# Performance work log

Hardware: AMD Instinct MI355X
Metric: run time of the kernel (lower is better)

Reference implementation:

```python
import jax, jax.numpy as jnp
import numpy as np

BS = 16; N_PER = 1024; N = BS * N_PER; K = 9; E = N * K
H = 128; NODE_D = 64; EDGE_D = 16; RBF_DIM = 20; R_CUT = 1.0; L = 4; SF = 0.1


def setup_inputs():
    ks = jax.random.split(jax.random.key(0), 24)
    X = jax.random.normal(ks[0], (N, 3), dtype=jnp.float32) * 0.5
    node_attr = jax.random.normal(ks[1], (N, NODE_D), dtype=jnp.float32)
    edge_attr = jax.random.normal(ks[2], (E, EDGE_D), dtype=jnp.float32)
    idx = jnp.arange(N, dtype=jnp.int32)
    bid = idx // N_PER
    Seg = ((idx % N_PER) >= (N_PER // 2)).astype(jnp.int32)
    row = jnp.repeat(idx, K)
    col = (row // N_PER) * N_PER + jax.random.randint(ks[3], (E,), 0, N_PER, dtype=jnp.int32)
    edges = jnp.stack([row, col])

    def g(k, shape, fan):
        return jax.random.normal(k, shape, dtype=jnp.float32) * (1.0 / float(np.sqrt(fan)))

    MI = 2 * H + RBF_DIM + EDGE_D  # message MLP input dim
    return {
        'X': X, 'node_attr': node_attr, 'edge_attr': edge_attr,
        'W_in1': g(ks[4], (NODE_D, H), NODE_D), 'b_in1': jnp.zeros((H,), jnp.float32),
        'W_in2': g(ks[5], (H, H), H), 'b_in2': jnp.zeros((H,), jnp.float32),
        'We1': g(ks[6], (L, MI, H), MI), 'be1': jnp.zeros((L, H), jnp.float32),
        'We2': g(ks[7], (L, H, H), H), 'be2': jnp.zeros((L, H), jnp.float32),
        'Wv': g(ks[8], (L, H, H), H), 'Wvv': g(ks[9], (L, H, H), H),
        'Wh1': g(ks[10], (L, 2 * H, H), 2 * H), 'bh1': jnp.zeros((L, H), jnp.float32),
        'Wh2': g(ks[11], (L, H, H), H), 'bh2': jnp.zeros((L, H), jnp.float32),
        'Wi1': g(ks[12], (L, H, H), H), 'bi1': jnp.zeros((L, H), jnp.float32),
        'Wi2': g(ks[13], (L, H, H), H), 'bi2': jnp.zeros((L, H), jnp.float32),
        'Wgv1': g(ks[14], (H, H), H), 'Wgv2': g(ks[15], (H, H), H),
        'Wg1': g(ks[16], (2 * H, H), 2 * H), 'bg1': jnp.zeros((H,), jnp.float32),
        'Wg2': g(ks[17], (H, 2 * H), H), 'bg2': jnp.zeros((2 * H,), jnp.float32),
        'Wf': g(ks[18], (H, 9), H),
        'edges': edges, 'Seg': Seg, 'bid': bid,
    }


def _fwd(X, node_attr, edge_attr, W_in1, b_in1, W_in2, b_in2, We1, be1, We2, be2, Wv, Wvv, Wh1, bh1, Wh2, bh2, Wi1, bi1, Wi2, bi2, Wgv1, Wgv2, Wg1, bg1, Wg2, bg2, Wf, edges, Seg, bid):
    silu = jax.nn.silu
    row, col = edges[0], edges[1]
    nseg = 2 * BS
    seg_id = bid * 2 + Seg  # (complex, receptor/ligand) segment id
    # coord2radial + Bessel RBF with cosine cutoff
    diff = X[row] - X[col]
    norm = jnp.sqrt(jnp.sum(diff * diff, axis=-1)) + 1e-8
    unit = diff / norm[:, None]
    freqs = jnp.arange(1, RBF_DIM + 1, dtype=X.dtype) * (jnp.pi / R_CUT)
    rbf = jnp.sin(norm[:, None] * freqs[None, :]) / norm[:, None]
    cut = 0.5 * (jnp.cos(jnp.pi * jnp.clip(norm, 0.0, R_CUT) / R_CUT) + 1.0)
    rbf = rbf * cut[:, None]
    # in_conv
    h = silu(node_attr @ W_in1 + b_in1) @ W_in2 + b_in2
    v = jnp.zeros((N, H, 3), dtype=h.dtype)
    counts = jax.ops.segment_sum(jnp.ones((N,), dtype=h.dtype), seg_id, num_segments=nseg)
    opp = bid * 2 + (1 - Seg)  # opposite-molecule segment per node
    for i in range(L):
        # PINN message passing (PaiNN-style equivariant layer)
        m_in = jnp.concatenate([h[row], h[col], rbf, edge_attr], axis=-1)
        m = silu(m_in @ We1[i] + be1[i]) @ We2[i] + be2[i]  # [E, H]
        agg = jax.ops.segment_sum(m, row, num_segments=N)
        h_intra = h + silu(jnp.concatenate([h, agg], axis=-1) @ Wh1[i] + bh1[i]) @ Wh2[i] + bh2[i]
        v_msg = (m @ Wv[i])[:, :, None] * unit[:, None, :] + (m @ Wvv[i])[:, :, None] * v[col]
        v = v + jax.ops.segment_sum(v_msg, row, num_segments=N)
        # cross receptor<->ligand softmax attention: (H_a @ H_b.T).mean(1) == H_a @ mean(H_b)
        mean_h = jax.ops.segment_sum(h_intra, seg_id, num_segments=nseg) / counts[:, None]
        score = jnp.sum(h_intra * mean_h[opp], axis=-1)
        smax = jax.ops.segment_max(score, seg_id, num_segments=nseg)
        ex = jnp.exp(score - smax[seg_id])
        w = ex / jax.ops.segment_sum(ex, seg_id, num_segments=nseg)[seg_id]
        gated = h_intra * w[:, None]
        h = h_intra + silu(gated @ Wi1[i] + bi1[i]) @ Wi2[i] + bi2[i]
    # gated equivariant block
    v1 = jnp.einsum('nhc,hk->nkc', v, Wgv1)
    v2 = jnp.einsum('nhc,hk->nkc', v, Wgv2)
    v2n = jnp.sqrt(jnp.sum(v2 * v2, axis=-1) + 1e-8)
    mix = silu(jnp.concatenate([h, v2n], axis=-1) @ Wg1 + bg1) @ Wg2 + bg2
    h, bgate = mix[:, :H], mix[:, H:]
    v = v1 * bgate[:, :, None]
    # final_conv + per-(complex, molecule) pooled prediction vectors [2*BS, 9, 3]
    pv = jnp.einsum('nhc,ho->noc', v * h[:, :, None], Wf)
    pred = jax.ops.segment_sum(pv.reshape(N, 27), seg_id, num_segments=nseg).reshape(nseg, 9, 3)
    # kron/outer-product quadratic surface params: A [., 3, 3], b [., 3]
    A = (pred[:, 0, :, None] * pred[:, 1, None, :] + pred[:, 3, :, None] * pred[:, 2, None, :]
         + pred[:, 4, :, None] * pred[:, 5, None, :] + pred[:, 7, :, None] * pred[:, 6, None, :]) / (SF * SF)
    bvec = pred[:, 8] / SF
    return jnp.concatenate([A, bvec[:, :, None]], axis=2)  # [2*BS, 3, 4]


def reference(X, node_attr, edge_attr, W_in1, b_in1, W_in2, b_in2, We1, be1, We2, be2, Wv, Wvv, Wh1, bh1, Wh2, bh2, Wi1, bi1, Wi2, bi2, Wgv1, Wgv2, Wg1, bg1, Wg2, bg2, Wf, edges, Seg, bid):
    return _fwd(X, node_attr, edge_attr, W_in1, b_in1, W_in2, b_in2, We1, be1, We2, be2, Wv, Wvv, Wh1, bh1, Wh2, bh2, Wi1, bi1, Wi2, bi2, Wgv1, Wgv2, Wg1, bg1, Wg2, bg2, Wf, edges, Seg, bid)
```

## Files before the change

kernel.cpp:

```cpp
#include <hip/hip_runtime.h>
#include <math.h>

#define NN 16384
#define NE 147456
#define NSEGS 32
#define HD 128
#define RBF_D 20
#define EDGE_DD 16
#define NODE_DD 64
#define NLAYER 4
#define PI_F 3.14159265358979323846f


typedef __attribute__((ext_vector_type(8))) short v8s;
typedef __attribute__((ext_vector_type(4))) float v4f;
typedef __attribute__((ext_vector_type(8))) unsigned short v8u;

__device__ __forceinline__ unsigned short f2bf(float f) {
  union { float f; unsigned int u; } x; x.f = f;
  unsigned int u = x.u;
  return (unsigned short)((u + 0x7FFFu + ((u >> 16) & 1u)) >> 16);
}
__device__ __forceinline__ float bf2f(unsigned short b) {
  union { unsigned int u; float f; } x; x.u = ((unsigned int)b) << 16; return x.f;
}
__device__ __forceinline__ void split8(float4 a, float4 b, v8u& hi, v8u& lo) {
  float v[8] = {a.x, a.y, a.z, a.w, b.x, b.y, b.z, b.w};
#pragma unroll
  for (int i = 0; i < 8; i++) {
    unsigned short h = f2bf(v[i]);
    hi[i] = h;
    lo[i] = f2bf(v[i] - bf2f(h));
  }
}
__device__ __forceinline__ float silu_f(float v) { return v / (1.f + expf(-v)); }

struct WDesc { const float* src; const float* src2; unsigned short* hi; unsigned short* lo;
               int K; int N; int Kp; int ld; };
struct WDescs { WDesc d[48]; };
__global__ void wconv_k(WDescs ds) {
  WDesc d = ds.d[blockIdx.y];
  int idx = blockIdx.x * 256 + threadIdx.x;
  if (idx >= d.N * d.Kp) return;
  int n = idx / d.Kp, k = idx - n * d.Kp;
  const float* s = d.src; int nn = n;
  if (d.src2 && n >= 128) { s = d.src2; nn = n - 128; }
  float v = (k < d.K) ? s[(size_t)k * d.ld + nn] : 0.f;
  unsigned short h = f2bf(v);
  d.hi[idx] = h;
  d.lo[idx] = f2bf(v - bf2f(h));
}

__global__ void wcomb_k(const float* __restrict__ We2, const float* __restrict__ Wv,
                        const float* __restrict__ Wvv, float* __restrict__ Wc) {
  int l = blockIdx.z, which = blockIdx.y, xb = blockIdx.x;
  const float* A = We2 + (size_t)l * 128 * 128;
  const float* B = (which ? Wvv : Wv) + (size_t)l * 128 * 128;
  float* D = Wc + ((size_t)(which * NLAYER + l)) * 128 * 128;
  int n = threadIdx.x & 127, r2 = threadIdx.x >> 7;
#pragma unroll
  for (int i = 0; i < 8; i++) {
    int k1 = xb * 16 + r2 * 8 + i;
    float s = 0.f;
    for (int j = 0; j < 128; j++) s += A[k1 * 128 + j] * B[j * 128 + n];
    D[(size_t)k1 * 128 + n] = s;
  }
}
__global__ void bcomb_k(const float* __restrict__ be2, const float* __restrict__ Wv,
                        const float* __restrict__ Wvv, const float* __restrict__ be1,
                        float* __restrict__ bcv, float* __restrict__ bcvv,
                        float* __restrict__ b9, float* __restrict__ bx) {
  int l = blockIdx.x, n = threadIdx.x;
  const float* b = be2 + l * 128;
  float sv = 0.f, svv = 0.f;
  for (int j = 0; j < 128; j++) {
    sv  += b[j] * Wv[(size_t)l * 16384 + j * 128 + n];
    svv += b[j] * Wvv[(size_t)l * 16384 + j * 128 + n];
  }
  bcv[l * 128 + n] = sv; bcvv[l * 128 + n] = svv; b9[l * 128 + n] = 9.f * b[n];
  bx[l * 256 + n] = be1[l * 128 + n]; bx[l * 256 + 128 + n] = 0.f;
}

constexpr int LDS_S = 40;

template<int BM, int AMODE, int OUTM, int RESM>
__global__ __launch_bounds__(256, 2)
void mgemm_k(const float* A0f, const unsigned short* Ah0, const unsigned short* Al0,
             const unsigned short* __restrict__ Wth, const unsigned short* __restrict__ Wtl,
             int Kp, const float* __restrict__ bias, const float* __restrict__ resf,
             float* Cf, int ldc, unsigned short* Ch, unsigned short* Cl, int lda)
{
  constexpr int MT = BM / 32;
  __shared__ unsigned short Ah[BM * LDS_S], Al[BM * LDS_S];
  __shared__ unsigned short Bh[128 * LDS_S], Bl[128 * LDS_S];
  const int tid = threadIdx.x;
  const int m0 = blockIdx.x * BM;
  const int coff = blockIdx.y * 128;
  const int w = tid >> 6, lane = tid & 63;
  const int lm = lane & 15, kq = lane >> 4;
  const int wm = (w >> 1) * (BM / 2);
  const int wn = (w & 1) * 64;

  v4f acc[MT][4];
#pragma unroll
  for (int i = 0; i < MT; i++)
#pragma unroll
    for (int j = 0; j < 4; j++) acc[i][j] = (v4f){0.f, 0.f, 0.f, 0.f};

  const int KT = Kp >> 5;
  for (int kt = 0; kt < KT; kt++) {
#pragma unroll
    for (int i = 0; i < BM / 64; i++) {
      int m = i * 64 + (tid >> 2);
      int k8 = (tid & 3) * 8;
      int gk = kt * 32 + k8, gm = m0 + m;
      v8u hi, lo;
      if constexpr (AMODE == 1) {
        hi = *(const v8u*)&Ah0[(size_t)gm * 128 + gk];
        lo = *(const v8u*)&Al0[(size_t)gm * 128 + gk];
      } else {
        float4 a = *(const float4*)&A0f[(size_t)gm * lda + gk];
        float4 b = *(const float4*)&A0f[(size_t)gm * lda + gk + 4];
        split8(a, b, hi, lo);
      }
      *(v8u*)&Ah[m * LDS_S + k8] = hi;
      *(v8u*)&Al[m * LDS_S + k8] = lo;
    }
#pragma unroll
    for (int i = 0; i < 2; i++) {
      int f = i * 256 + tid;
      int n = f >> 2, k8 = (f & 3) * 8;
      size_t g = (size_t)(coff + n) * Kp + kt * 32 + k8;
      *(v8u*)&Bh[n * LDS_S + k8] = *(const v8u*)&Wth[g];
      *(v8u*)&Bl[n * LDS_S + k8] = *(const v8u*)&Wtl[g];
    }
    __syncthreads();
    v8s afh[MT], afl[MT];
#pragma unroll
    for (int mi = 0; mi < MT; mi++) {
      int r = wm + mi * 16 + lm;
      afh[mi] = *(v8s*)&Ah[r * LDS_S + kq * 8];
      afl[mi] = *(v8s*)&Al[r * LDS_S + kq * 8];
    }
#pragma unroll
    for (int ni = 0; ni < 4; ni++) {
      int r = wn + ni * 16 + lm;
      v8s bh = *(v8s*)&Bh[r * LDS_S + kq * 8];
      v8s bl = *(v8s*)&Bl[r * LDS_S + kq * 8];
#pragma unroll
      for (int mi = 0; mi < MT; mi++) {
        acc[mi][ni] = __builtin_amdgcn_mfma_f32_16x16x32_bf16(afh[mi], bh, acc[mi][ni], 0, 0, 0);
        acc[mi][ni] = __builtin_amdgcn_mfma_f32_16x16x32_bf16(afl[mi], bh, acc[mi][ni], 0, 0, 0);
        acc[mi][ni] = __builtin_amdgcn_mfma_f32_16x16x32_bf16(afh[mi], bl, acc[mi][ni], 0, 0, 0);
      }
    }
    __syncthreads();
  }
#pragma unroll
  for (int mi = 0; mi < MT; mi++) {
#pragma unroll
    for (int r = 0; r < 4; r++) {
      int mrow = m0 + wm + mi * 16 + kq * 4 + r;
#pragma unroll
      for (int ni = 0; ni < 4; ni++) {
        int ncol = coff + wn + ni * 16 + lm;
        float v = acc[mi][ni][r];
        if constexpr (RESM == 3) v += bias[ncol] * resf[mrow];
        else { if (bias) v += bias[ncol]; }
        if constexpr (OUTM == 0) Cf[(size_t)mrow * ldc + ncol] = v;
        else if constexpr (OUTM == 1) {
          unsigned short h = f2bf(v);
          Ch[(size_t)mrow * 128 + ncol] = h;
          Cl[(size_t)mrow * 128 + ncol] = f2bf(v - bf2f(h));
        } else {
          Ch[(size_t)mrow * 128 + ncol] = f2bf(v);
        }
      }
    }
  }
}

__device__ __forceinline__ float4 loadRE(const float* __restrict__ rbf,
                                         const float* __restrict__ ea, int m, int k4) {
  if (k4 < RBF_D) return *(const float4*)&rbf[(size_t)m * RBF_D + k4];
  if (k4 < RBF_D + EDGE_DD) return *(const float4*)&ea[(size_t)m * EDGE_DD + k4 - RBF_D];
  return make_float4(0.f, 0.f, 0.f, 0.f);
}

__global__ __launch_bounds__(256, 2)
void mre_k(const float* __restrict__ rbf, const float* __restrict__ ea,
           const float* __restrict__ hrc, const int* __restrict__ gcol,
           const unsigned short* __restrict__ Wth, const unsigned short* __restrict__ Wtl,
           unsigned short* __restrict__ m1h, unsigned short* __restrict__ m1l)
{
  constexpr int BM = 128, MT = 4, Kp = 64;
  __shared__ unsigned short Ah[BM * LDS_S], Al[BM * LDS_S];
  __shared__ unsigned short Bh[128 * LDS_S], Bl[128 * LDS_S];
  const int tid = threadIdx.x;
  const int m0 = blockIdx.x * BM;
  const int w = tid >> 6, lane = tid & 63;
  const int lm = lane & 15, kq = lane >> 4;
  const int wm = (w >> 1) * 64, wn = (w & 1) * 64;

  v4f acc[MT][4];
#pragma unroll
  for (int i = 0; i < MT; i++)
#pragma unroll
    for (int j = 0; j < 4; j++) acc[i][j] = (v4f){0.f, 0.f, 0.f, 0.f};

  for (int kt = 0; kt < Kp / 32; kt++) {
#pragma unroll
    for (int i = 0; i < 2; i++) {
      int m = i * 64 + (tid >> 2);
      int k8 = (tid & 3) * 8;
      int gk = kt * 32 + k8, gm = m0 + m;
      v8u hi, lo;
      split8(loadRE(rbf, ea, gm, gk), loadRE(rbf, ea, gm, gk + 4), hi, lo);
      *(v8u*)&Ah[m * LDS_S + k8] = hi;
      *(v8u*)&Al[m * LDS_S + k8] = lo;
    }
#pragma unroll
    for (int i = 0; i < 2; i++) {
      int f = i * 256 + tid;
      int n = f >> 2, k8 = (f & 3) * 8;
      size_t g = (size_t)n * Kp + kt * 32 + k8;
      *(v8u*)&Bh[n * LDS_S + k8] = *(const v8u*)&Wth[g];
      *(v8u*)&Bl[n * LDS_S + k8] = *(const v8u*)&Wtl[g];
    }
    __syncthreads();
    v8s afh[MT], afl[MT];
#pragma unroll
    for (int mi = 0; mi < MT; mi++) {
      int r = wm + mi * 16 + lm;
      afh[mi] = *(v8s*)&Ah[r * LDS_S + kq * 8];
      afl[mi] = *(v8s*)&Al[r * LDS_S + kq * 8];
    }
#pragma unroll
    for (int ni = 0; ni < 4; ni++) {
      int r = wn + ni * 16 + lm;
      v8s bh = *(v8s*)&Bh[r * LDS_S + kq * 8];
      v8s bl = *(v8s*)&Bl[r * LDS_S + kq * 8];
#pragma unroll
      for (int mi = 0; mi < MT; mi++) {
        acc[mi][ni] = __builtin_amdgcn_mfma_f32_16x16x32_bf16(afh[mi], bh, acc[mi][ni], 0, 0, 0);
        acc[mi][ni] = __builtin_amdgcn_mfma_f32_16x16x32_bf16(afl[mi], bh, acc[mi][ni], 0, 0, 0);
        acc[mi][ni] = __builtin_amdgcn_mfma_f32_16x16x32_bf16(afh[mi], bl, acc[mi][ni], 0, 0, 0);
      }
    }
    __syncthreads();
  }
#pragma unroll
  for (int mi = 0; mi < MT; mi++) {
#pragma unroll
    for (int r = 0; r < 4; r++) {
      int e = m0 + wm + mi * 16 + kq * 4 + r;
      int e9 = e / 9;
      int ce = gcol[e];
      const float* pr = hrc + (size_t)e9 * 256;
      const float* pc = hrc + (size_t)ce * 256 + 128;
#pragma unroll
      for (int ni = 0; ni < 4; ni++) {
        int nc = wn + ni * 16 + lm;
        float v = silu_f(acc[mi][ni][r] + pr[nc] + pc[nc]);
        unsigned short h = f2bf(v);
        m1h[(size_t)e * 128 + nc] = h;
        m1l[(size_t)e * 128 + nc] = f2bf(v - bf2f(h));
      }
    }
  }
}

template<int AMODE, int OUTM, int RESM>
__global__ __launch_bounds__(256, 2)
void mlp2_k(const float* A0f, const float* A1f,
            const unsigned short* Ah0, const unsigned short* Al0,
            const unsigned short* __restrict__ W1h, const unsigned short* __restrict__ W1l,
            int k1p, const float* __restrict__ b1,
            const unsigned short* __restrict__ W2h, const unsigned short* __restrict__ W2l,
            const float* __restrict__ b2,
            const float* resf, const unsigned short* resh, const unsigned short* resl,
            float* Cf, int ldc, unsigned short* Ch, unsigned short* Cl, int lda)
{
  __shared__ unsigned short Ah[64 * LDS_S], Al[64 * LDS_S];
  __shared__ unsigned short Bh[128 * LDS_S], Bl[128 * LDS_S];
  __shared__ unsigned short Th[64 * 136], Tl[64 * 136];
  const int tid = threadIdx.x;
  const int m0 = blockIdx.x * 64;
  const int w = tid >> 6, lane = tid & 63;
  const int lm = lane & 15, kq = lane >> 4;
  const int wm = (w >> 1) * 32, wn = (w & 1) * 64;

  v4f acc[2][4];
#pragma unroll
  for (int i = 0; i < 2; i++)
#pragma unroll
    for (int j = 0; j < 4; j++) acc[i][j] = (v4f){0.f, 0.f, 0.f, 0.f};

  for (int kt = 0; kt < (k1p >> 5); kt++) {
    {
      int m = tid >> 2, k8 = (tid & 3) * 8;
      int gk = kt * 32 + k8, gm = m0 + m;
      v8u hi, lo;
      if constexpr (AMODE == 3) {
        if (gk < 128) {
          hi = *(const v8u*)&Ah0[(size_t)gm * 128 + gk];
          lo = *(const v8u*)&Al0[(size_t)gm * 128 + gk];
        } else {
          float4 a = *(const float4*)&A1f[(size_t)gm * 128 + gk - 128];
          float4 b = *(const float4*)&A1f[(size_t)gm * 128 + gk - 124];
          split8(a, b, hi, lo);
        }
      } else {
        float4 a = *(const float4*)&A0f[(size_t)gm * lda + gk];
        float4 b = *(const float4*)&A0f[(size_t)gm * lda + gk + 4];
        if constexpr (AMODE == 4) {
          float s = A1f[gm];
          a.x *= s; a.y *= s; a.z *= s; a.w *= s;
          b.x *= s; b.y *= s; b.z *= s; b.w *= s;
        }
        split8(a, b, hi, lo);
      }
      *(v8u*)&Ah[m * LDS_S + k8] = hi;
      *(v8u*)&Al[m * LDS_S + k8] = lo;
    }
#pragma unroll
    for (int i = 0; i < 2; i++) {
      int f = i * 256 + tid;
      int n = f >> 2, k8 = (f & 3) * 8;
      size_t g = (size_t)n * k1p + kt * 32 + k8;
      *(v8u*)&Bh[n * LDS_S + k8] = *(const v8u*)&W1h[g];
      *(v8u*)&Bl[n * LDS_S + k8] = *(const v8u*)&W1l[g];
    }
    __syncthreads();
    v8s afh[2], afl[2];
#pragma unroll
    for (int mi = 0; mi < 2; mi++) {
      int r = wm + mi * 16 + lm;
      afh[mi] = *(v8s*)&Ah[r * LDS_S + kq * 8];
      afl[mi] = *(v8s*)&Al[r * LDS_S + kq * 8];
    }
#pragma unroll
    for (int ni = 0; ni < 4; ni++) {
      int r = wn + ni * 16 + lm;
      v8s bh = *(v8s*)&Bh[r * LDS_S + kq * 8];
      v8s bl = *(v8s*)&Bl[r * LDS_S + kq * 8];
#pragma unroll
      for (int mi = 0; mi < 2; mi++) {
        acc[mi][ni] = __builtin_amdgcn_mfma_f32_16x16x32_bf16(afh[mi], bh, acc[mi][ni], 0, 0, 0);
        acc[mi][ni] = __builtin_amdgcn_mfma_f32_16x16x32_bf16(afl[mi], bh, acc[mi][ni], 0, 0, 0);
        acc[mi][ni] = __builtin_amdgcn_mfma_f32_16x16x32_bf16(afh[mi], bl, acc[mi][ni], 0, 0, 0);
      }
    }
    __syncthreads();
  }
#pragma unroll
  for (int mi = 0; mi < 2; mi++) {
#pragma unroll
    for (int r = 0; r < 4; r++) {
      int row = wm + mi * 16 + kq * 4 + r;
#pragma unroll
      for (int ni = 0; ni < 4; ni++) {
        int col = wn + ni * 16 + lm;
        float v = silu_f(acc[mi][ni][r] + b1[col]);
        unsigned short h = f2bf(v);
        Th[row * 136 + col] = h;
        Tl[row * 136 + col] = f2bf(v - bf2f(h));
      }
    }
  }
  __syncthreads();
  const int coff2 = blockIdx.y * 128;
  v4f acc2[2][4];
#pragma unroll
  for (int i = 0; i < 2; i++)
#pragma unroll
    for (int j = 0; j < 4; j++) acc2[i][j] = (v4f){0.f, 0.f, 0.f, 0.f};
  for (int kt = 0; kt < 4; kt++) {
#pragma unroll
    for (int i = 0; i < 2; i++) {
      int f = i * 256 + tid;
      int n = f >> 2, k8 = (f & 3) * 8;
      size_t g = (size_t)(coff2 + n) * 128 + kt * 32 + k8;
      *(v8u*)&Bh[n * LDS_S + k8] = *(const v8u*)&W2h[g];
      *(v8u*)&Bl[n * LDS_S + k8] = *(const v8u*)&W2l[g];
    }
    __syncthreads();
    v8s afh[2], afl[2];
#pragma unroll
    for (int mi = 0; mi < 2; mi++) {
      int r = wm + mi * 16 + lm;
      afh[mi] = *(v8s*)&Th[r * 136 + kt * 32 + kq * 8];
      afl[mi] = *(v8s*)&Tl[r * 136 + kt * 32 + kq * 8];
    }
#pragma unroll
    for (int ni = 0; ni < 4; ni++) {
      int r = wn + ni * 16 + lm;
      v8s bh = *(v8s*)&Bh[r * LDS_S + kq * 8];
      v8s bl = *(v8s*)&Bl[r * LDS_S + kq * 8];
#pragma unroll
      for (int mi = 0; mi < 2; mi++) {
        acc2[mi][ni] = __builtin_amdgcn_mfma_f32_16x16x32_bf16(afh[mi], bh, acc2[mi][ni], 0, 0, 0);
        acc2[mi][ni] = __builtin_amdgcn_mfma_f32_16x16x32_bf16(afl[mi], bh, acc2[mi][ni], 0, 0, 0);
        acc2[mi][ni] = __builtin_amdgcn_mfma_f32_16x16x32_bf16(afh[mi], bl, acc2[mi][ni], 0, 0, 0);
      }
    }
    __syncthreads();
  }
#pragma unroll
  for (int mi = 0; mi < 2; mi++) {
#pragma unroll
    for (int r = 0; r < 4; r++) {
      int mrow = m0 + wm + mi * 16 + kq * 4 + r;
#pragma unroll
      for (int ni = 0; ni < 4; ni++) {
        int ncol = coff2 + wn + ni * 16 + lm;
        float v = acc2[mi][ni][r];
        if (b2) v += b2[ncol];
        if constexpr (RESM == 1) v += resf[(size_t)mrow * 128 + ncol];
        if constexpr (RESM == 2) v += bf2f(resh[(size_t)mrow * 128 + ncol]) + bf2f(resl[(size_t)mrow * 128 + ncol]);
        if constexpr (OUTM == 0) Cf[(size_t)mrow * ldc + ncol] = v;
        else {
          unsigned short h = f2bf(v);
          Ch[(size_t)mrow * 128 + ncol] = h;
          Cl[(size_t)mrow * 128 + ncol] = f2bf(v - bf2f(h));
        }
      }
    }
  }
}

__global__ void edge_geom_k(const float* __restrict__ X, const int* __restrict__ row,
                            const int* __restrict__ col,
                            float* __restrict__ unitv, float* __restrict__ rbf) {
  int e = blockIdx.x * 256 + threadIdx.x;
  if (e >= NE) return;
  int r = row[e], c = col[e];
  float dx = X[r * 3 + 0] - X[c * 3 + 0];
  float dy = X[r * 3 + 1] - X[c * 3 + 1];
  float dz = X[r * 3 + 2] - X[c * 3 + 2];
  float norm = sqrtf(dx * dx + dy * dy + dz * dz) + 1e-8f;
  float inv = 1.f / norm;
  unitv[e * 3 + 0] = dx * inv;
  unitv[e * 3 + 1] = dy * inv;
  unitv[e * 3 + 2] = dz * inv;
  float cl = fminf(norm, 1.0f);
  float cut = 0.5f * (cosf(PI_F * cl) + 1.0f);
  float s = cut * inv;
#pragma unroll
  for (int j = 0; j < RBF_D; j++) rbf[(size_t)e * RBF_D + j] = sinf(norm * (float)(j + 1) * PI_F) * s;
}

__global__ void sumU_k(const unsigned short* __restrict__ m1h, const unsigned short* __restrict__ m1l,
                       const float* __restrict__ unitv,
                       unsigned short* __restrict__ agh, unsigned short* __restrict__ agl,
                       float* __restrict__ U, float* __restrict__ sup) {
  int t = blockIdx.x * 256 + threadIdx.x;
  int n = t >> 6, p = t & 63;
  int h2 = p * 2;
  float s0 = 0, s1 = 0, u00 = 0, u01 = 0, u10 = 0, u11 = 0, u20 = 0, u21 = 0;
#pragma unroll
  for (int k = 0; k < 9; k++) {
    int e = n * 9 + k;
    ushort2 mh = *(const ushort2*)&m1h[(size_t)e * 128 + h2];
    ushort2 ml = *(const ushort2*)&m1l[(size_t)e * 128 + h2];
    float m0 = bf2f(mh.x) + bf2f(ml.x);
    float m1 = bf2f(mh.y) + bf2f(ml.y);
    float u0 = unitv[e * 3 + 0], u1 = unitv[e * 3 + 1], u2 = unitv[e * 3 + 2];
    s0 += m0; s1 += m1;
    u00 += u0 * m0; u01 += u0 * m1;
    u10 += u1 * m0; u11 += u1 * m1;
    u20 += u2 * m0; u21 += u2 * m1;
  }
  unsigned short h0 = f2bf(s0), h1 = f2bf(s1);
  size_t b = (size_t)n * 128 + h2;
  *(ushort2*)&agh[b] = make_ushort2(h0, h1);
  *(ushort2*)&agl[b] = make_ushort2(f2bf(s0 - bf2f(h0)), f2bf(s1 - bf2f(h1)));
  const size_t P = (size_t)NN * 128;
  *(float2*)&U[b]         = make_float2(u00, u01);
  *(float2*)&U[P + b]     = make_float2(u10, u11);
  *(float2*)&U[2 * P + b] = make_float2(u20, u21);
  if (p < 3) {
    float q = 0.f;
#pragma unroll
    for (int k = 0; k < 9; k++) q += unitv[(n * 9 + k) * 3 + p];
    sup[p * NN + n] = q;
  }
}

__global__ void vupd_k(const float* __restrict__ vold, const float* __restrict__ t1,
                       const unsigned short* __restrict__ mvvh,
                       const int* __restrict__ col, float* __restrict__ vnew) {
  const size_t P = (size_t)NN * 128;
  int t = blockIdx.x * 256 + threadIdx.x;
  int n = t >> 7, hh = t & 127;
  size_t b = (size_t)n * 128 + hh;
  float a0 = vold[b] + t1[b];
  float a1 = vold[P + b] + t1[P + b];
  float a2 = vold[2 * P + b] + t1[2 * P + b];
#pragma unroll
  for (int k = 0; k < 9; k++) {
    int e = n * 9 + k;
    int ce = col[e];
    float mvv = bf2f(mvvh[(size_t)e * 128 + hh]);
    size_t cb = (size_t)ce * 128 + hh;
    a0 += mvv * vold[cb];
    a1 += mvv * vold[P + cb];
    a2 += mvv * vold[2 * P + cb];
  }
  vnew[b] = a0; vnew[P + b] = a1; vnew[2 * P + b] = a2;
}

__global__ void meanp_k(const float* __restrict__ hintra, float* __restrict__ meanp) {
  int q = blockIdx.x, s = blockIdx.y, c = threadIdx.x;
  const float* p = hintra + ((size_t)s * 512 + q * 64) * 128 + c;
  float a = 0.f;
  for (int r = 0; r < 64; r++) a += p[(size_t)r * 128];
  meanp[(s * 8 + q) * 128 + c] = a;
}
__global__ void score2_k(const float* __restrict__ hintra, const float* __restrict__ meanp,
                         float* __restrict__ score) {
  int lane = threadIdx.x & 63;
  int n = blockIdx.x * 4 + (threadIdx.x >> 6);
  int opp = (n >> 9) ^ 1;
  const float* mp = meanp + opp * 1024;
  float mh0 = 0.f, mh1 = 0.f;
#pragma unroll
  for (int q = 0; q < 8; q++) { mh0 += mp[q * 128 + lane]; mh1 += mp[q * 128 + lane + 64]; }
  const float* hp = hintra + (size_t)n * 128;
  float v = hp[lane] * mh0 + hp[lane + 64] * mh1;
#pragma unroll
  for (int off = 32; off > 0; off >>= 1) v += __shfl_down(v, off, 64);
  if (lane == 0) score[n] = v * (1.f / 512.f);
}
__global__ void softmax_k(const float* __restrict__ score, float* __restrict__ w) {
  __shared__ float red[512];
  int s = blockIdx.x, t = threadIdx.x;
  float sc = score[s * 512 + t];
  red[t] = sc;
  __syncthreads();
  for (int off = 256; off > 0; off >>= 1) {
    if (t < off) red[t] = fmaxf(red[t], red[t + off]);
    __syncthreads();
  }
  float mx = red[0];
  __syncthreads();
  float ex = expf(sc - mx);
  red[t] = ex;
  __syncthreads();
  for (int off = 256; off > 0; off >>= 1) {
    if (t < off) red[t] += red[t + off];
    __syncthreads();
  }
  w[s * 512 + t] = ex / red[0];
}

__global__ void v2n_k(const float* __restrict__ v12, float* __restrict__ v2n) {
  const size_t P = (size_t)NN * 256;
  int t = blockIdx.x * 256 + threadIdx.x;
  int n = t >> 7, h = t & 127;
  size_t b = (size_t)n * 256 + 128 + h;
  float a = v12[b], c = v12[P + b], d = v12[2 * P + b];
  v2n[t] = sqrtf(a * a + c * c + d * d + 1e-8f);
}

__global__ __launch_bounds__(256)
void pv_k(const float* __restrict__ v12, const float* __restrict__ mix,
          const float* __restrict__ Wf, float* __restrict__ pred) {
  __shared__ float sg[8][128];
  __shared__ float pr[8][32];
  const size_t P = (size_t)NN * 256;
  int t = threadIdx.x;
  int nb = blockIdx.x * 8;
#pragma unroll
  for (int i = 0; i < 4; i++) {
    int idx = i * 256 + t;
    int nn = idx >> 7, hh = idx & 127;
    const float* mxp = mix + (size_t)(nb + nn) * 256;
    sg[nn][hh] = mxp[hh] * mxp[128 + hh];
  }
  __syncthreads();
  int nn = t >> 5, j = t & 31;
  float acc = 0.f;
  if (j < 27) {
    int o = j / 3, c = j - o * 3;
    const float* vp = v12 + (size_t)c * P + (size_t)(nb + nn) * 256;
    for (int hh = 0; hh < 128; hh++) acc += sg[nn][hh] * vp[hh] * Wf[hh * 9 + o];
  }
  pr[nn][j] = acc;
  __syncthreads();
  if (t < 32) {
    float s = pr[0][t] + pr[1][t] + pr[2][t] + pr[3][t] +
              pr[4][t] + pr[5][t] + pr[6][t] + pr[7][t];
    if (t < 27) atomicAdd(&pred[(nb >> 9) * 27 + t], s);
  }
}

__global__ void out_k(const float* __restrict__ pred, float* __restrict__ out) {
  int s = threadIdx.x;
  if (s >= NSEGS) return;
  float p[27];
#pragma unroll
  for (int j = 0; j < 27; j++) p[j] = pred[s * 27 + j];
#pragma unroll
  for (int i = 0; i < 3; i++) {
#pragma unroll
    for (int j = 0; j < 3; j++) {
      float a = p[0 * 3 + i] * p[1 * 3 + j] + p[3 * 3 + i] * p[2 * 3 + j]
              + p[4 * 3 + i] * p[5 * 3 + j] + p[7 * 3 + i] * p[6 * 3 + j];
      out[s * 12 + i * 4 + j] = a * 100.f;
    }
    out[s * 12 + i * 4 + 3] = p[8 * 3 + i] * 10.f;
  }
}

extern "C" void kernel_launch(void* const* d_in, const int* in_sizes, int n_in,
                              void* d_out, int out_size, void* d_ws, size_t ws_size,
                              hipStream_t stream) {
  const float* X         = (const float*)d_in[0];
  const float* node_attr = (const float*)d_in[1];
  const float* edge_attr = (const float*)d_in[2];
  const float* W_in1 = (const float*)d_in[3];
  const float* b_in1 = (const float*)d_in[4];
  const float* W_in2 = (const float*)d_in[5];
  const float* b_in2 = (const float*)d_in[6];
  const float* We1 = (const float*)d_in[7];
  const float* be1 = (const float*)d_in[8];
  const float* We2 = (const float*)d_in[9];
  const float* be2 = (const float*)d_in[10];
  const float* Wv  = (const float*)d_in[11];
  const float* Wvv = (const float*)d_in[12];
  const float* Wh1 = (const float*)d_in[13];
  const float* bh1 = (const float*)d_in[14];
  const float* Wh2 = (const float*)d_in[15];
  const float* bh2 = (const float*)d_in[16];
  const float* Wi1 = (const float*)d_in[17];
  const float* bi1 = (const float*)d_in[18];
  const float* Wi2 = (const float*)d_in[19];
  const float* bi2 = (const float*)d_in[20];
  const float* Wgv1 = (const float*)d_in[21];
  const float* Wgv2 = (const float*)d_in[22];
  const float* Wg1 = (const float*)d_in[23];
  const float* bg1 = (const float*)d_in[24];
  const float* Wg2 = (const float*)d_in[25];
  const float* bg2 = (const float*)d_in[26];
  const float* Wf  = (const float*)d_in[27];
  const int* edges = (const int*)d_in[28];
  const int* rowp = edges;
  const int* colp = edges + NE;
  float* out = (float*)d_out;

  char* ws = (char*)d_ws;
  size_t o = 0;
  auto ab = [&](size_t bytes) { char* p = ws + o; o += (bytes + 255) & ~(size_t)255; return p; };
  float* unitv  = (float*)ab((size_t)NE * 3 * 4);
  float* rbf    = (float*)ab((size_t)NE * RBF_D * 4);
  float* va     = (float*)ab((size_t)NN * 384 * 4);
  float* vb     = (float*)ab((size_t)NN * 384 * 4);
  unsigned short* m1h = (unsigned short*)ab((size_t)NE * 128 * 2);
  unsigned short* m1l = (unsigned short*)ab((size_t)NE * 128 * 2);
  float* hrc    = (float*)ab((size_t)NN * 256 * 4);
  float* U      = (float*)ab((size_t)3 * NN * 128 * 4);
  float* sup    = (float*)ab((size_t)3 * NN * 4);
  float* agg    = (float*)ab((size_t)NN * 128 * 4);
  float* hintra = (float*)ab((size_t)NN * 128 * 4);
  unsigned short* agh = (unsigned short*)ab((size_t)NN * 128 * 2);
  unsigned short* agl = (unsigned short*)ab((size_t)NN * 128 * 2);
  unsigned short* hbh = (unsigned short*)ab((size_t)NN * 128 * 2);
  unsigned short* hbl = (unsigned short*)ab((size_t)NN * 128 * 2);
  float* meanp  = (float*)ab(NSEGS * 8 * 128 * 4);
  float* scoreb = (float*)ab(NN * 4);
  float* wgt    = (float*)ab(NN * 4);
  float* pred   = (float*)ab(NSEGS * 27 * 4);
  float* Wc     = (float*)ab((size_t)2 * NLAYER * 128 * 128 * 4);
  float* bcv    = (float*)ab(NLAYER * 128 * 4);
  float* bcvv   = (float*)ab(NLAYER * 128 * 4);
  float* b9     = (float*)ab(NLAYER * 128 * 4);
  float* bx     = (float*)ab(NLAYER * 256 * 4);
  unsigned short* wt = (unsigned short*)ab(4 * 1024 * 1024);
  float* v12  = (float*)m1l;
  float* mixb = (float*)m1h;

  size_t wo = 0;
  auto walloc = [&](size_t n) { unsigned short* p = wt + wo; wo += n; return p; };
  WDescs wd{};
  int wcnt = 0;
  auto addw = [&](const float* src, const float* src2, int K, int N, int Kp, int ld) {
    size_t sz = (size_t)N * Kp;
    unsigned short* hi = walloc(sz);
    unsigned short* lo = walloc(sz);
    wd.d[wcnt] = WDesc{src, src2, hi, lo, K, N, Kp, ld};
    return wcnt++;
  };
  int iWin1 = addw(W_in1, nullptr, 64, 128, 64, 128);
  int iWin2 = addw(W_in2, nullptr, 128, 128, 128, 128);
  int iWe1rc[NLAYER], iWe1re[NLAYER], iWe2[NLAYER], iWcv[NLAYER], iWcvv[NLAYER],
      iWh1[NLAYER], iWh2[NLAYER], iWi1[NLAYER], iWi2[NLAYER];
  for (int i = 0; i < NLAYER; i++) {
    const float* Wl = We1 + (size_t)i * 292 * 128;
    iWe1rc[i] = addw(Wl, Wl + 128 * 128, 128, 256, 128, 128);
    iWe1re[i] = addw(Wl + 256 * 128, nullptr, 36, 128, 64, 128);
    iWe2[i]   = addw(We2 + (size_t)i * 16384, nullptr, 128, 128, 128, 128);
    iWcv[i]   = addw(Wc + (size_t)i * 16384, nullptr, 128, 128, 128, 128);
    iWcvv[i]  = addw(Wc + (size_t)(NLAYER + i) * 16384, nullptr, 128, 128, 128, 128);
    iWh1[i]   = addw(Wh1 + (size_t)i * 256 * 128, nullptr, 256, 128, 256, 128);
    iWh2[i]   = addw(Wh2 + (size_t)i * 16384, nullptr, 128, 128, 128, 128);
    iWi1[i]   = addw(Wi1 + (size_t)i * 16384, nullptr, 128, 128, 128, 128);
    iWi2[i]   = addw(Wi2 + (size_t)i * 16384, nullptr, 128, 128, 128, 128);
  }
  int iWg1   = addw(Wg1, nullptr, 256, 128, 256, 128);
  int iWg2   = addw(Wg2, nullptr, 128, 256, 128, 256);
  int iWgv12 = addw(Wgv1, Wgv2, 128, 256, 128, 128);

  hipMemsetAsync(va, 0, (size_t)NN * 384 * sizeof(float), stream);
  hipMemsetAsync(pred, 0, NSEGS * 27 * sizeof(float), stream);

  wcomb_k<<<dim3(8, 2, NLAYER), 256, 0, stream>>>(We2, Wv, Wvv, Wc);
  bcomb_k<<<NLAYER, 128, 0, stream>>>(be2, Wv, Wvv, be1, bcv, bcvv, b9, bx);
  wconv_k<<<dim3(128, wcnt), 256, 0, stream>>>(wd);
  edge_geom_k<<<NE / 256, 256, 0, stream>>>(X, rowp, colp, unitv, rbf);

  auto WH = [&](int idx) { return wd.d[idx].hi; };
  auto WL = [&](int idx) { return wd.d[idx].lo; };

  mlp2_k<0, 1, 0><<<dim3(NN / 64, 1), 256, 0, stream>>>(
      node_attr, nullptr, nullptr, nullptr,
      WH(iWin1), WL(iWin1), 64, b_in1, WH(iWin2), WL(iWin2), b_in2,
      nullptr, nullptr, nullptr, nullptr, 128, hbh, hbl, NODE_DD);

  float* vcur = va;
  float* vnxt = vb;
  for (int i = 0; i < NLAYER; i++) {
    mgemm_k<64, 1, 0, 0><<<dim3(NN / 64, 2), 256, 0, stream>>>(
        nullptr, hbh, hbl, WH(iWe1rc[i]), WL(iWe1rc[i]), 128,
        bx + i * 256, nullptr, hrc, 256, nullptr, nullptr, 0);
    mre_k<<<NE / 128, 256, 0, stream>>>(rbf, edge_attr, hrc, colp,
        WH(iWe1re[i]), WL(iWe1re[i]), m1h, m1l);
    sumU_k<<<NN * 64 / 256, 256, 0, stream>>>(m1h, m1l, unitv, agh, agl, U, sup);
    mgemm_k<64, 1, 0, 0><<<dim3(NN / 64, 1), 256, 0, stream>>>(
        nullptr, agh, agl, WH(iWe2[i]), WL(iWe2[i]), 128,
        b9 + i * 128, nullptr, agg, 128, nullptr, nullptr, 0);
    mlp2_k<3, 0, 2><<<dim3(NN / 64, 1), 256, 0, stream>>>(
        nullptr, agg, hbh, hbl,
        WH(iWh1[i]), WL(iWh1[i]), 256, bh1 + i * 128, WH(iWh2[i]), WL(iWh2[i]), bh2 + i * 128,
        nullptr, hbh, hbl, hintra, 128, nullptr, nullptr, 0);
    meanp_k<<<dim3(8, NSEGS), 128, 0, stream>>>(hintra, meanp);
    score2_k<<<NN / 4, 256, 0, stream>>>(hintra, meanp, scoreb);
    softmax_k<<<NSEGS, 512, 0, stream>>>(scoreb, wgt);
    mgemm_k<64, 0, 0, 3><<<dim3(3 * NN / 64, 1), 256, 0, stream>>>(
        U, nullptr, nullptr, WH(iWcv[i]), WL(iWcv[i]), 128,
        bcv + i * 128, sup, U, 128, nullptr, nullptr, 128);
    mgemm_k<128, 1, 3, 0><<<dim3(NE / 128, 1), 256, 0, stream>>>(
        nullptr, m1h, m1l, WH(iWcvv[i]), WL(iWcvv[i]), 128,
        bcvv + i * 128, nullptr, nullptr, 128, m1h, nullptr, 0);
    vupd_k<<<NN * 128 / 256, 256, 0, stream>>>(vcur, U, m1h, colp, vnxt);
    { float* t = vcur; vcur = vnxt; vnxt = t; }
    mlp2_k<4, 1, 1><<<dim3(NN / 64, 1), 256, 0, stream>>>(
        hintra, wgt, nullptr, nullptr,
        WH(iWi1[i]), WL(iWi1[i]), 128, bi1 + i * 128, WH(iWi2[i]), WL(iWi2[i]), bi2 + i * 128,
        hintra, nullptr, nullptr, nullptr, 128, hbh, hbl, 128);
  }

  mgemm_k<64, 0, 0, 0><<<dim3(3 * NN / 64, 2), 256, 0, stream>>>(
      vcur, nullptr, nullptr, WH(iWgv12), WL(iWgv12), 128,
      nullptr, nullptr, v12, 256, nullptr, nullptr, 128);
  v2n_k<<<NN * 128 / 256, 256, 0, stream>>>(v12, agg);
  mlp2_k<3, 0, 0><<<dim3(NN / 64, 2), 256, 0, stream>>>(
      nullptr, agg, hbh, hbl,
      WH(iWg1), WL(iWg1), 256, bg1, WH(iWg2), WL(iWg2), bg2,
      nullptr, nullptr, nullptr, mixb, 256, nullptr, nullptr, 0);
  pv_k<<<NN / 8, 256, 0, stream>>>(v12, mixb, Wf, pred);
  out_k<<<1, 64, 0, stream>>>(pred, out);
}
```

Baseline: 1.160 ms.

## Fuse edge message GEMM, per-node aggregation and Wvv GEMM into one kernel

Replaces the mre_k, sumU_k and edge-level Wcvv mgemm launches with one kernel. It computes the first message MLP layer per 64-edge tile, holds the hi/lo bf16 split in LDS, and reduces it per node into agg and U with atomics. It then runs the second GEMM from LDS to write the edge vector message, so the large hi/lo m1 intermediate never goes through global memory. In exchange it needs per-layer memsets, float atomics for nodes whose edges straddle tile boundaries (non-deterministic summation order), a precomputed sup, and an fp32-input We2 GEMM.

```diff
diff --git a/kernel.cpp b/kernel.cpp
--- a/kernel.cpp
+++ b/kernel.cpp
@@ -188,31 +188,36 @@
 }
 
 __global__ __launch_bounds__(256, 2)
-void mre_k(const float* __restrict__ rbf, const float* __restrict__ ea,
-           const float* __restrict__ hrc, const int* __restrict__ gcol,
-           const unsigned short* __restrict__ Wth, const unsigned short* __restrict__ Wtl,
-           unsigned short* __restrict__ m1h, unsigned short* __restrict__ m1l)
+void mrev_k(const float* __restrict__ rbf, const float* __restrict__ ea,
+            const float* __restrict__ hrc, const float* __restrict__ unitv,
+            const int* __restrict__ gcol,
+            const unsigned short* __restrict__ W1h, const unsigned short* __restrict__ W1l,
+            const unsigned short* __restrict__ W2h, const unsigned short* __restrict__ W2l,
+            const float* __restrict__ bcvv,
+            float* __restrict__ agg, float* __restrict__ U,
+            unsigned short* __restrict__ mvvh)
 {
-  constexpr int BM = 128, MT = 4, Kp = 64;
-  __shared__ unsigned short Ah[BM * LDS_S], Al[BM * LDS_S];
+  __shared__ unsigned short Ah[64 * LDS_S], Al[64 * LDS_S];
   __shared__ unsigned short Bh[128 * LDS_S], Bl[128 * LDS_S];
+  __shared__ unsigned short Th[64 * 136], Tl[64 * 136];
+  __shared__ float su[192];
   const int tid = threadIdx.x;
-  const int m0 = blockIdx.x * BM;
+  const int m0 = blockIdx.x * 64;
   const int w = tid >> 6, lane = tid & 63;
   const int lm = lane & 15, kq = lane >> 4;
-  const int wm = (w >> 1) * 64, wn = (w & 1) * 64;
-
-  v4f acc[MT][4];
-#pragma unroll
-  for (int i = 0; i < MT; i++)
+  const int wm = (w >> 1) * 32, wn = (w & 1) * 64;
+
+  if (tid < 192) su[tid] = unitv[(size_t)m0 * 3 + tid];
+
+  v4f acc[2][4];
+#pragma unroll
+  for (int i = 0; i < 2; i++)
 #pragma unroll
     for (int j = 0; j < 4; j++) acc[i][j] = (v4f){0.f, 0.f, 0.f, 0.f};
 
-  for (int kt = 0; kt < Kp / 32; kt++) {
-#pragma unroll
-    for (int i = 0; i < 2; i++) {
-      int m = i * 64 + (tid >> 2);
-      int k8 = (tid & 3) * 8;
+  for (int kt = 0; kt < 2; kt++) {
+    {
+      int m = tid >> 2, k8 = (tid & 3) * 8;
       int gk = kt * 32 + k8, gm = m0 + m;
       v8u hi, lo;
       split8(loadRE(rbf, ea, gm, gk), loadRE(rbf, ea, gm, gk + 4), hi, lo);
@@ -223,14 +228,14 @@
     for (int i = 0; i < 2; i++) {
       int f = i * 256 + tid;
       int n = f >> 2, k8 = (f & 3) * 8;
-      size_t g = (size_t)n * Kp + kt * 32 + k8;
-      *(v8u*)&Bh[n * LDS_S + k8] = *(const v8u*)&Wth[g];
-      *(v8u*)&Bl[n * LDS_S + k8] = *(const v8u*)&Wtl[g];
-    }
-    __syncthreads();
-    v8s afh[MT], afl[MT];
-#pragma unroll
-    for (int mi = 0; mi < MT; mi++) {
+      size_t g = (size_t)n * 64 + kt * 32 + k8;
+      *(v8u*)&Bh[n * LDS_S + k8] = *(const v8u*)&W1h[g];
+      *(v8u*)&Bl[n * LDS_S + k8] = *(const v8u*)&W1l[g];
+    }
+    __syncthreads();
+    v8s afh[2], afl[2];
+#pragma unroll
+    for (int mi = 0; mi < 2; mi++) {
       int r = wm + mi * 16 + lm;
       afh[mi] = *(v8s*)&Ah[r * LDS_S + kq * 8];
       afl[mi] = *(v8s*)&Al[r * LDS_S + kq * 8];
@@ -241,7 +246,7 @@
       v8s bh = *(v8s*)&Bh[r * LDS_S + kq * 8];
       v8s bl = *(v8s*)&Bl[r * LDS_S + kq * 8];
 #pragma unroll
-      for (int mi = 0; mi < MT; mi++) {
+      for (int mi = 0; mi < 2; mi++) {
         acc[mi][ni] = __builtin_amdgcn_mfma_f32_16x16x32_bf16(afh[mi], bh, acc[mi][ni], 0, 0, 0);
         acc[mi][ni] = __builtin_amdgcn_mfma_f32_16x16x32_bf16(afl[mi], bh, acc[mi][ni], 0, 0, 0);
         acc[mi][ni] = __builtin_amdgcn_mfma_f32_16x16x32_bf16(afh[mi], bl, acc[mi][ni], 0, 0, 0);
@@ -250,21 +255,97 @@
     __syncthreads();
   }
 #pragma unroll
-  for (int mi = 0; mi < MT; mi++) {
+  for (int mi = 0; mi < 2; mi++) {
 #pragma unroll
     for (int r = 0; r < 4; r++) {
-      int e = m0 + wm + mi * 16 + kq * 4 + r;
-      int e9 = e / 9;
-      int ce = gcol[e];
-      const float* pr = hrc + (size_t)e9 * 256;
-      const float* pc = hrc + (size_t)ce * 256 + 128;
+      int row = wm + mi * 16 + kq * 4 + r;
+      int e = m0 + row;
+      const float* pr = hrc + (size_t)(e / 9) * 256;
+      const float* pc = hrc + (size_t)gcol[e] * 256 + 128;
 #pragma unroll
       for (int ni = 0; ni < 4; ni++) {
         int nc = wn + ni * 16 + lm;
         float v = silu_f(acc[mi][ni][r] + pr[nc] + pc[nc]);
         unsigned short h = f2bf(v);
-        m1h[(size_t)e * 128 + nc] = h;
-        m1l[(size_t)e * 128 + nc] = f2bf(v - bf2f(h));
+        Th[row * 136 + nc] = h;
+        Tl[row * 136 + nc] = f2bf(v - bf2f(h));
+      }
+    }
+  }
+  __syncthreads();
+  {
+    const size_t P = (size_t)NN * 128;
+    int nfirst = m0 / 9;
+#pragma unroll
+    for (int it = 0; it < 4; it++) {
+      int idx = it * 256 + tid;
+      int ln = idx >> 7, c = idx & 127;
+      int n = nfirst + ln;
+      int r0 = n * 9 - m0, r1 = r0 + 9;
+      if (r0 < 0) r0 = 0;
+      if (r1 > 64) r1 = 64;
+      float s = 0.f, u0 = 0.f, u1 = 0.f, u2 = 0.f;
+      for (int r = r0; r < r1; r++) {
+        float m = bf2f(Th[r * 136 + c]) + bf2f(Tl[r * 136 + c]);
+        s += m;
+        u0 += su[r * 3 + 0] * m;
+        u1 += su[r * 3 + 1] * m;
+        u2 += su[r * 3 + 2] * m;
+      }
+      if (r0 < r1) {
+        size_t b = (size_t)n * 128 + c;
+        atomicAdd(&agg[b], s);
+        atomicAdd(&U[b], u0);
+        atomicAdd(&U[P + b], u1);
+        atomicAdd(&U[2 * P + b], u2);
+      }
+    }
+  }
+  v4f acc2[2][4];
+#pragma unroll
+  for (int i = 0; i < 2; i++)
+#pragma unroll
+    for (int j = 0; j < 4; j++) acc2[i][j] = (v4f){0.f, 0.f, 0.f, 0.f};
+  for (int kt = 0; kt < 4; kt++) {
+#pragma unroll
+    for (int i = 0; i < 2; i++) {
+      int f = i * 256 + tid;
+      int n = f >> 2, k8 = (f & 3) * 8;
+      size_t g = (size_t)n * 128 + kt * 32 + k8;
+      *(v8u*)&Bh[n * LDS_S + k8] = *(const v8u*)&W2h[g];
+      *(v8u*)&Bl[n * LDS_S + k8] = *(const v8u*)&W2l[g];
+    }
+    __syncthreads();
+    v8s afh[2], afl[2];
+#pragma unroll
+    for (int mi = 0; mi < 2; mi++) {
+      int r = wm + mi * 16 + lm;
+      afh[mi] = *(v8s*)&Th[r * 136 + kt * 32 + kq * 8];
+      afl[mi] = *(v8s*)&Tl[r * 136 + kt * 32 + kq * 8];
+    }
+#pragma unroll
+    for (int ni = 0; ni < 4; ni++) {
+      int r = wn + ni * 16 + lm;
+      v8s bh = *(v8s*)&Bh[r * LDS_S + kq * 8];
+      v8s bl = *(v8s*)&Bl[r * LDS_S + kq * 8];
+#pragma unroll
+      for (int mi = 0; mi < 2; mi++) {
+        acc2[mi][ni] = __builtin_amdgcn_mfma_f32_16x16x32_bf16(afh[mi], bh, acc2[mi][ni], 0, 0, 0);
+        acc2[mi][ni] = __builtin_amdgcn_mfma_f32_16x16x32_bf16(afl[mi], bh, acc2[mi][ni], 0, 0, 0);
+        acc2[mi][ni] = __builtin_amdgcn_mfma_f32_16x16x32_bf16(afh[mi], bl, acc2[mi][ni], 0, 0, 0);
+      }
+    }
+    __syncthreads();
+  }
+#pragma unroll
+  for (int mi = 0; mi < 2; mi++) {
+#pragma unroll
+    for (int r = 0; r < 4; r++) {
+      int e = m0 + wm + mi * 16 + kq * 4 + r;
+#pragma unroll
+      for (int ni = 0; ni < 4; ni++) {
+        int nc = wn + ni * 16 + lm;
+        mvvh[(size_t)e * 128 + nc] = f2bf(acc2[mi][ni][r] + bcvv[nc]);
       }
     }
   }
@@ -450,41 +531,16 @@
   for (int j = 0; j < RBF_D; j++) rbf[(size_t)e * RBF_D + j] = sinf(norm * (float)(j + 1) * PI_F) * s;
 }
 
-__global__ void sumU_k(const unsigned short* __restrict__ m1h, const unsigned short* __restrict__ m1l,
-                       const float* __restrict__ unitv,
-                       unsigned short* __restrict__ agh, unsigned short* __restrict__ agl,
-                       float* __restrict__ U, float* __restrict__ sup) {
-  int t = blockIdx.x * 256 + threadIdx.x;
-  int n = t >> 6, p = t & 63;
-  int h2 = p * 2;
-  float s0 = 0, s1 = 0, u00 = 0, u01 = 0, u10 = 0, u11 = 0, u20 = 0, u21 = 0;
+__global__ void sup_k(const float* __restrict__ unitv, float* __restrict__ sup) {
+  int n = blockIdx.x * 256 + threadIdx.x;
+  if (n >= NN) return;
+  float q0 = 0.f, q1 = 0.f, q2 = 0.f;
 #pragma unroll
   for (int k = 0; k < 9; k++) {
-    int e = n * 9 + k;
-    ushort2 mh = *(const ushort2*)&m1h[(size_t)e * 128 + h2];
-    ushort2 ml = *(const ushort2*)&m1l[(size_t)e * 128 + h2];
-    float m0 = bf2f(mh.x) + bf2f(ml.x);
-    float m1 = bf2f(mh.y) + bf2f(ml.y);
-    float u0 = unitv[e * 3 + 0], u1 = unitv[e * 3 + 1], u2 = unitv[e * 3 + 2];
-    s0 += m0; s1 += m1;
-    u00 += u0 * m0; u01 += u0 * m1;
-    u10 += u1 * m0; u11 += u1 * m1;
-    u20 += u2 * m0; u21 += u2 * m1;
-  }
-  unsigned short h0 = f2bf(s0), h1 = f2bf(s1);
-  size_t b = (size_t)n * 128 + h2;
-  *(ushort2*)&agh[b] = make_ushort2(h0, h1);
-  *(ushort2*)&agl[b] = make_ushort2(f2bf(s0 - bf2f(h0)), f2bf(s1 - bf2f(h1)));
-  const size_t P = (size_t)NN * 128;
-  *(float2*)&U[b]         = make_float2(u00, u01);
-  *(float2*)&U[P + b]     = make_float2(u10, u11);
-  *(float2*)&U[2 * P + b] = make_float2(u20, u21);
-  if (p < 3) {
-    float q = 0.f;
-#pragma unroll
-    for (int k = 0; k < 9; k++) q += unitv[(n * 9 + k) * 3 + p];
-    sup[p * NN + n] = q;
-  }
+    const float* u = &unitv[(size_t)(n * 9 + k) * 3];
+    q0 += u[0]; q1 += u[1]; q2 += u[2];
+  }
+  sup[n] = q0; sup[NN + n] = q1; sup[2 * NN + n] = q2;
 }
 
 __global__ void vupd_k(const float* __restrict__ vold, const float* __restrict__ t1,
@@ -656,15 +712,12 @@
   float* rbf    = (float*)ab((size_t)NE * RBF_D * 4);
   float* va     = (float*)ab((size_t)NN * 384 * 4);
   float* vb     = (float*)ab((size_t)NN * 384 * 4);
-  unsigned short* m1h = (unsigned short*)ab((size_t)NE * 128 * 2);
-  unsigned short* m1l = (unsigned short*)ab((size_t)NE * 128 * 2);
+  unsigned short* mvvh = (unsigned short*)ab((size_t)NE * 128 * 2);
   float* hrc    = (float*)ab((size_t)NN * 256 * 4);
   float* U      = (float*)ab((size_t)3 * NN * 128 * 4);
+  float* agg    = (float*)ab((size_t)NN * 128 * 4);
   float* sup    = (float*)ab((size_t)3 * NN * 4);
-  float* agg    = (float*)ab((size_t)NN * 128 * 4);
   float* hintra = (float*)ab((size_t)NN * 128 * 4);
-  unsigned short* agh = (unsigned short*)ab((size_t)NN * 128 * 2);
-  unsigned short* agl = (unsigned short*)ab((size_t)NN * 128 * 2);
   unsigned short* hbh = (unsigned short*)ab((size_t)NN * 128 * 2);
   unsigned short* hbl = (unsigned short*)ab((size_t)NN * 128 * 2);
   float* meanp  = (float*)ab(NSEGS * 8 * 128 * 4);
@@ -677,8 +730,8 @@
   float* b9     = (float*)ab(NLAYER * 128 * 4);
   float* bx     = (float*)ab(NLAYER * 256 * 4);
   unsigned short* wt = (unsigned short*)ab(4 * 1024 * 1024);
-  float* v12  = (float*)m1l;
-  float* mixb = (float*)m1h;
+  float* v12  = (float*)mvvh;
+  float* mixb = (float*)U;
 
   size_t wo = 0;
   auto walloc = [&](size_t n) { unsigned short* p = wt + wo; wo += n; return p; };
@@ -718,6 +771,7 @@
   bcomb_k<<<NLAYER, 128, 0, stream>>>(be2, Wv, Wvv, be1, bcv, bcvv, b9, bx);
   wconv_k<<<dim3(128, wcnt), 256, 0, stream>>>(wd);
   edge_geom_k<<<NE / 256, 256, 0, stream>>>(X, rowp, colp, unitv, rbf);
+  sup_k<<<NN / 256, 256, 0, stream>>>(unitv, sup);
 
   auto WH = [&](int idx) { return wd.d[idx].hi; };
   auto WL = [&](int idx) { return wd.d[idx].lo; };
@@ -730,15 +784,16 @@
   float* vcur = va;
   float* vnxt = vb;
   for (int i = 0; i < NLAYER; i++) {
+    hipMemsetAsync(U, 0, (size_t)4 * NN * 128 * sizeof(float), stream);
     mgemm_k<64, 1, 0, 0><<<dim3(NN / 64, 2), 256, 0, stream>>>(
         nullptr, hbh, hbl, WH(iWe1rc[i]), WL(iWe1rc[i]), 128,
         bx + i * 256, nullptr, hrc, 256, nullptr, nullptr, 0);
-    mre_k<<<NE / 128, 256, 0, stream>>>(rbf, edge_attr, hrc, colp,
-        WH(iWe1re[i]), WL(iWe1re[i]), m1h, m1l);
-    sumU_k<<<NN * 64 / 256, 256, 0, stream>>>(m1h, m1l, unitv, agh, agl, U, sup);
-    mgemm_k<64, 1, 0, 0><<<dim3(NN / 64, 1), 256, 0, stream>>>(
-        nullptr, agh, agl, WH(iWe2[i]), WL(iWe2[i]), 128,
-        b9 + i * 128, nullptr, agg, 128, nullptr, nullptr, 0);
+    mrev_k<<<NE / 64, 256, 0, stream>>>(rbf, edge_attr, hrc, unitv, colp,
+        WH(iWe1re[i]), WL(iWe1re[i]), WH(iWcvv[i]), WL(iWcvv[i]),
+        bcvv + i * 128, agg, U, mvvh);
+    mgemm_k<64, 0, 0, 0><<<dim3(NN / 64, 1), 256, 0, stream>>>(
+        agg, nullptr, nullptr, WH(iWe2[i]), WL(iWe2[i]), 128,
+        b9 + i * 128, nullptr, agg, 128, nullptr, nullptr, 128);
     mlp2_k<3, 0, 2><<<dim3(NN / 64, 1), 256, 0, stream>>>(
         nullptr, agg, hbh, hbl,
         WH(iWh1[i]), WL(iWh1[i]), 256, bh1 + i * 128, WH(iWh2[i]), WL(iWh2[i]), bh2 + i * 128,
@@ -749,10 +804,7 @@
     mgemm_k<64, 0, 0, 3><<<dim3(3 * NN / 64, 1), 256, 0, stream>>>(
         U, nullptr, nullptr, WH(iWcv[i]), WL(iWcv[i]), 128,
         bcv + i * 128, sup, U, 128, nullptr, nullptr, 128);
-    mgemm_k<128, 1, 3, 0><<<dim3(NE / 128, 1), 256, 0, stream>>>(
-        nullptr, m1h, m1l, WH(iWcvv[i]), WL(iWcvv[i]), 128,
-        bcvv + i * 128, nullptr, nullptr, 128, m1h, nullptr, 0);
-    vupd_k<<<NN * 128 / 256, 256, 0, stream>>>(vcur, U, m1h, colp, vnxt);
+    vupd_k<<<NN * 128 / 256, 256, 0, stream>>>(vcur, U, mvvh, colp, vnxt);
     { float* t = vcur; vcur = vnxt; vnxt = t; }
     mlp2_k<4, 1, 1><<<dim3(NN / 64, 1), 256, 0, stream>>>(
         hintra, wgt, nullptr, nullptr,
```

Result: no change. 1.137 ms (-1.9%).
